# Kernel optimization log

Hardware: AMD Instinct MI355X
Metric: run time of the kernel (lower is better)

## Reference

```python
import jax, jax.numpy as jnp
import numpy as np

L, H, B = 16, 1024, 4096


def setup_inputs() -> dict:
    key = jax.random.key(0)
    k1, k2, k3, k4 = jax.random.split(key, 4)
    z = jax.random.normal(k1, (B, H), dtype=jnp.float32)
    layer_ids = jax.random.randint(k2, (B,), 0, L)
    # Module initializes weight = identity per layer; add small noise so the
    # transform is non-trivial while staying near the module's init regime.
    eye = jnp.broadcast_to(jnp.eye(H, dtype=jnp.float32), (L, H, H))
    weight = eye + 0.02 * jax.random.normal(k3, (L, H, H), dtype=jnp.float32)
    bias = 0.02 * jax.random.normal(k4, (L, H), dtype=jnp.float32)
    return {"z": z, "layer_ids": layer_ids, "weight": weight, "bias": bias}


def reference(z, layer_ids, weight, bias):
    # Faithful math: out[b] = weight[layer_ids[b]] @ z[b] + bias[layer_ids[b]].
    # Instead of materializing the gathered [B,H,H] weight tensor (as torch.bmm
    # forces), compute all-layer outputs with a grouped GEMM [B,L,H] and select.
    out_all = jnp.einsum('lij,bj->bli', weight, z)  # [B, L, H]
    out = jnp.take_along_axis(out_all, layer_ids[:, None, None], axis=1)[:, 0, :]  # [B, H]
    return out + bias[layer_ids]
```

## Files before the change

kernel.cpp:

```cpp
#include <hip/hip_runtime.h>


#define HDIM 1024
#define LNUM 16
#define BTOT 4096

constexpr int BM = 64, BN = 128, BK = 32;
constexpr int NT = HDIM / BK;
constexpr int MSLOTS = 8;

constexpr int LROW = 128;
constexpr int AOFF = 0;
constexpr int BOFF = 8192;
constexpr int BUFSZ = 24576;

typedef __attribute__((ext_vector_type(4))) float floatx4;
typedef __attribute__((ext_vector_type(2))) __fp16 cvt16x2;
typedef __attribute__((ext_vector_type(8))) _Float16 f16x8;
typedef __attribute__((ext_vector_type(2))) unsigned int uintx2;

__device__ __forceinline__ void split4(floatx4 v, uintx2& hw, uintx2& lw) {
    cvt16x2 h01 = __builtin_amdgcn_cvt_pkrtz(v[0], v[1]);
    cvt16x2 h23 = __builtin_amdgcn_cvt_pkrtz(v[2], v[3]);
    cvt16x2 l01 = __builtin_amdgcn_cvt_pkrtz(v[0] - (float)h01[0],
                                             v[1] - (float)h01[1]);
    cvt16x2 l23 = __builtin_amdgcn_cvt_pkrtz(v[2] - (float)h23[0],
                                             v[3] - (float)h23[1]);
    hw[0] = __builtin_bit_cast(unsigned int, h01);
    hw[1] = __builtin_bit_cast(unsigned int, h23);
    lw[0] = __builtin_bit_cast(unsigned int, l01);
    lw[1] = __builtin_bit_cast(unsigned int, l23);
}

__global__ __launch_bounds__(256, 3) void fused_grouped_mfma_kernel(
    const float* __restrict__ z,
    const int* __restrict__ layer_ids,
    const float* __restrict__ weight,
    const float* __restrict__ bias,
    float* __restrict__ out) {

    const int bid  = blockIdx.x;
    const int xcd  = bid & 7;
    const int slot = bid >> 3;
    const int l    = xcd + ((slot >> 6) << 3);
    const int rem  = slot & 63;
    const int my   = rem >> 3;
    const int nx   = rem & 7;
    const int n0   = nx * BN;

    const int tid  = threadIdx.x;
    const int lane = tid & 63;
    const int w    = tid >> 6;
    const int wm   = w & 1;
    const int wn   = w >> 1;

    __shared__ __align__(16) unsigned char sm[2][BUFSZ];
    __shared__ int permTile[BM];
    __shared__ int waveSums[4];

    const int4* lid4 = (const int4*)layer_ids;
    unsigned mask = 0;
#pragma unroll
    for (int q = 0; q < 4; ++q) {
        int4 v = lid4[tid * 4 + q];
        mask |= (unsigned)(v.x == l) << (4 * q)
             |  (unsigned)(v.y == l) << (4 * q + 1)
             |  (unsigned)(v.z == l) << (4 * q + 2)
             |  (unsigned)(v.w == l) << (4 * q + 3);
    }
    const int ct = __popc(mask);
    int x = ct;
#pragma unroll
    for (int o = 1; o < 64; o <<= 1) {
        int v = __shfl_up(x, o);
        if (lane >= o) x += v;
    }
    if (lane == 63) waveSums[w] = x;
    __syncthreads();
    int waveBase = 0, cnt = 0;
#pragma unroll
    for (int w2 = 0; w2 < 4; ++w2) {
        int s = waveSums[w2];
        if (w2 < w) waveBase += s;
        cnt += s;
    }
    const int et = waveBase + x - ct;

    const int kq  = tid & 7;
    const int rb  = tid >> 3;
    const int swz = (rb & 7) << 1;
    const int wA_hi = AOFF + rb * LROW + ((kq ^ swz) << 3);
    const int wA_lo = AOFF + rb * LROW + (((8 + kq) ^ swz) << 3);
    const int wB_hi = BOFF + rb * LROW + ((kq ^ swz) << 3);
    const int wB_lo = BOFF + rb * LROW + (((8 + kq) ^ swz) << 3);

    const int lr = lane & 15;
    const int ks = lane >> 4;
    const int rdA_hi = AOFF + (wm * 32 + lr) * LROW + ((ks ^ (lr & 7)) << 4);
    const int rdA_lo = AOFF + (wm * 32 + lr) * LROW + (((4 + ks) ^ (lr & 7)) << 4);
    const int rdB_hi = BOFF + (wn * 64 + lr) * LROW + ((ks ^ (lr & 7)) << 4);
    const int rdB_lo = BOFF + (wn * 64 + lr) * LROW + (((4 + ks) ^ (lr & 7)) << 4);

    const float* wBase = weight + (size_t)l * HDIM * HDIM;
    const int colBase = n0 + wn * 64 + lr;
    float bb[4];
#pragma unroll
    for (int j = 0; j < 4; ++j) bb[j] = bias[l * HDIM + colBase + j * 16];

    for (int m0 = my * BM; m0 < cnt; m0 += MSLOTS * BM) {
        __syncthreads();
        {
            unsigned m2 = mask;
            int r = et;
            while (m2) {
                int p = __ffs(m2) - 1;
                m2 &= m2 - 1;
                unsigned rr = (unsigned)(r - m0);
                if (rr < (unsigned)BM) permTile[rr] = tid * 16 + p;
                ++r;
            }
        }
        __syncthreads();

        const float* aPtr[2];
        const float* bPtr[4];
#pragma unroll
        for (int p = 0; p < 2; ++p) {
            int gm = rb + 32 * p;
            if (gm > cnt - 1 - m0) gm = cnt - 1 - m0;
            aPtr[p] = z + (size_t)permTile[gm] * HDIM + kq * 4;
        }
#pragma unroll
        for (int p = 0; p < 4; ++p)
            bPtr[p] = wBase + (size_t)(n0 + rb + 32 * p) * HDIM + kq * 4;

        floatx4 acc[2][4] = {};
        floatx4 av[2], bv[4];

        auto loadT = [&](int k0) {
#pragma unroll
            for (int p = 0; p < 2; ++p) av[p] = *(const floatx4*)(aPtr[p] + k0);
#pragma unroll
            for (int p = 0; p < 4; ++p) bv[p] = *(const floatx4*)(bPtr[p] + k0);
        };

        auto stageT = [&](unsigned char* buf) {
            uintx2 hw, lw;
#pragma unroll
            for (int p = 0; p < 2; ++p) {
                split4(av[p], hw, lw);
                *(uintx2*)(buf + wA_hi + p * 4096) = hw;
                *(uintx2*)(buf + wA_lo + p * 4096) = lw;
            }
#pragma unroll
            for (int p = 0; p < 4; ++p) {
                split4(bv[p], hw, lw);
                *(uintx2*)(buf + wB_hi + p * 4096) = hw;
                *(uintx2*)(buf + wB_lo + p * 4096) = lw;
            }
        };

        auto compute = [&](const unsigned char* buf) {
            f16x8 ah[2], al[2], bh[4], bl[4];
#pragma unroll
            for (int i = 0; i < 2; ++i) {
                ah[i] = *(const f16x8*)(buf + rdA_hi + i * 2048);
                al[i] = *(const f16x8*)(buf + rdA_lo + i * 2048);
            }
#pragma unroll
            for (int j = 0; j < 4; ++j) {
                bh[j] = *(const f16x8*)(buf + rdB_hi + j * 2048);
                bl[j] = *(const f16x8*)(buf + rdB_lo + j * 2048);
            }
#pragma unroll
            for (int i = 0; i < 2; ++i)
#pragma unroll
                for (int j = 0; j < 4; ++j) {
                    acc[i][j] = __builtin_amdgcn_mfma_f32_16x16x32_f16(
                        ah[i], bh[j], acc[i][j], 0, 0, 0);
                    acc[i][j] = __builtin_amdgcn_mfma_f32_16x16x32_f16(
                        ah[i], bl[j], acc[i][j], 0, 0, 0);
                    acc[i][j] = __builtin_amdgcn_mfma_f32_16x16x32_f16(
                        al[i], bh[j], acc[i][j], 0, 0, 0);
                }
        };

        loadT(0);
        stageT(sm[0]);
        __syncthreads();

#pragma unroll 1
        for (int t2 = 0; t2 < NT; t2 += 2) {
            loadT((t2 + 1) * BK);
            compute(sm[0]);
            stageT(sm[1]);
            __syncthreads();
            if (t2 + 2 < NT) {
                loadT((t2 + 2) * BK);
                compute(sm[1]);
                stageT(sm[0]);
                __syncthreads();
            } else {
                compute(sm[1]);
            }
        }

        const int rq = lane >> 4;
#pragma unroll
        for (int i = 0; i < 2; ++i) {
#pragma unroll
            for (int v = 0; v < 4; ++v) {
                int gm = wm * 32 + i * 16 + rq * 4 + v;
                if (m0 + gm < cnt) {
                    float* o = out + (size_t)permTile[gm] * HDIM + colBase;
#pragma unroll
                    for (int j = 0; j < 4; ++j) o[j * 16] = acc[i][j][v] + bb[j];
                }
            }
        }
    }
}

extern "C" void kernel_launch(void* const* d_in, const int* in_sizes, int n_in,
                              void* d_out, int out_size, void* d_ws, size_t ws_size,
                              hipStream_t stream) {
    const float* z = nullptr;
    const int* layer_ids = nullptr;
    const float* weight = nullptr;
    const float* bias = nullptr;
    for (int i = 0; i < n_in; ++i) {
        switch (in_sizes[i]) {
            case BTOT * HDIM:        z = (const float*)d_in[i]; break;
            case BTOT:               layer_ids = (const int*)d_in[i]; break;
            case LNUM * HDIM * HDIM: weight = (const float*)d_in[i]; break;
            case LNUM * HDIM:        bias = (const float*)d_in[i]; break;
        }
    }
    float* out = (float*)d_out;

    fused_grouped_mfma_kernel<<<dim3(1024), 256, 0, stream>>>(
        z, layer_ids, weight, bias, out);
}
```

Measured before the change: 146.1 us.

## Load MFMA operands directly from global memory, drop LDS staging and weight lo term

Removes the shared-memory double buffer and its barriers. Each lane now loads its MFMA fragments straight from global memory and converts them to fp16 in registers. The weight operand is rounded to a single fp16 value, dropping its low-order correction term, so each k-step issues two MFMAs per tile instead of three. Occupancy hint is lowered to 2. The change removes LDS traffic and synchronization, but it also loses the LDS reuse across waves, so each wave re-fetches its own A/B rows from global/L2. It also lowers accuracy, because the weight is now single-fp16 precision.

Measured after the change: 220.8 us. +51.2%, slower.

```diff
diff --git a/kernel.cpp b/kernel.cpp
--- a/kernel.cpp
+++ b/kernel.cpp
@@ -8,16 +8,12 @@
 constexpr int BM = 64, BN = 128, BK = 32;
 constexpr int NT = HDIM / BK;
 constexpr int MSLOTS = 8;
-
-constexpr int LROW = 128;
-constexpr int AOFF = 0;
-constexpr int BOFF = 8192;
-constexpr int BUFSZ = 24576;
 
 typedef __attribute__((ext_vector_type(4))) float floatx4;
 typedef __attribute__((ext_vector_type(2))) __fp16 cvt16x2;
 typedef __attribute__((ext_vector_type(8))) _Float16 f16x8;
 typedef __attribute__((ext_vector_type(2))) unsigned int uintx2;
+typedef __attribute__((ext_vector_type(4))) unsigned int uintx4;
 
 __device__ __forceinline__ void split4(floatx4 v, uintx2& hw, uintx2& lw) {
     cvt16x2 h01 = __builtin_amdgcn_cvt_pkrtz(v[0], v[1]);
@@ -32,7 +28,31 @@
     lw[1] = __builtin_bit_cast(unsigned int, l23);
 }
 
-__global__ __launch_bounds__(256, 3) void fused_grouped_mfma_kernel(
+__device__ __forceinline__ void split8(floatx4 v0, floatx4 v1,
+                                       f16x8& hi, f16x8& lo) {
+    uintx2 h0, l0, h1, l1;
+    split4(v0, h0, l0);
+    split4(v1, h1, l1);
+    uintx4 h = {h0[0], h0[1], h1[0], h1[1]};
+    uintx4 l = {l0[0], l0[1], l1[0], l1[1]};
+    hi = __builtin_bit_cast(f16x8, h);
+    lo = __builtin_bit_cast(f16x8, l);
+}
+
+__device__ __forceinline__ f16x8 cvt8_rtn(floatx4 v0, floatx4 v1) {
+    unsigned u0 = (unsigned)__builtin_bit_cast(unsigned short, (_Float16)v0[0])
+                | ((unsigned)__builtin_bit_cast(unsigned short, (_Float16)v0[1]) << 16);
+    unsigned u1 = (unsigned)__builtin_bit_cast(unsigned short, (_Float16)v0[2])
+                | ((unsigned)__builtin_bit_cast(unsigned short, (_Float16)v0[3]) << 16);
+    unsigned u2 = (unsigned)__builtin_bit_cast(unsigned short, (_Float16)v1[0])
+                | ((unsigned)__builtin_bit_cast(unsigned short, (_Float16)v1[1]) << 16);
+    unsigned u3 = (unsigned)__builtin_bit_cast(unsigned short, (_Float16)v1[2])
+                | ((unsigned)__builtin_bit_cast(unsigned short, (_Float16)v1[3]) << 16);
+    uintx4 u = {u0, u1, u2, u3};
+    return __builtin_bit_cast(f16x8, u);
+}
+
+__global__ __launch_bounds__(256, 2) void fused_direct_mfma_kernel(
     const float* __restrict__ z,
     const int* __restrict__ layer_ids,
     const float* __restrict__ weight,
@@ -54,7 +74,6 @@
     const int wm   = w & 1;
     const int wn   = w >> 1;
 
-    __shared__ __align__(16) unsigned char sm[2][BUFSZ];
     __shared__ int permTile[BM];
     __shared__ int waveSums[4];
 
@@ -86,22 +105,15 @@
     }
     const int et = waveBase + x - ct;
 
-    const int kq  = tid & 7;
-    const int rb  = tid >> 3;
-    const int swz = (rb & 7) << 1;
-    const int wA_hi = AOFF + rb * LROW + ((kq ^ swz) << 3);
-    const int wA_lo = AOFF + rb * LROW + (((8 + kq) ^ swz) << 3);
-    const int wB_hi = BOFF + rb * LROW + ((kq ^ swz) << 3);
-    const int wB_lo = BOFF + rb * LROW + (((8 + kq) ^ swz) << 3);
-
     const int lr = lane & 15;
     const int ks = lane >> 4;
-    const int rdA_hi = AOFF + (wm * 32 + lr) * LROW + ((ks ^ (lr & 7)) << 4);
-    const int rdA_lo = AOFF + (wm * 32 + lr) * LROW + (((4 + ks) ^ (lr & 7)) << 4);
-    const int rdB_hi = BOFF + (wn * 64 + lr) * LROW + ((ks ^ (lr & 7)) << 4);
-    const int rdB_lo = BOFF + (wn * 64 + lr) * LROW + (((4 + ks) ^ (lr & 7)) << 4);
-
     const float* wBase = weight + (size_t)l * HDIM * HDIM;
+
+    const float* bRow[4];
+#pragma unroll
+    for (int j = 0; j < 4; ++j)
+        bRow[j] = wBase + (size_t)(n0 + wn * 64 + j * 16 + lr) * HDIM + ks * 8;
+
     const int colBase = n0 + wn * 64 + lr;
     float bb[4];
 #pragma unroll
@@ -122,87 +134,54 @@
         }
         __syncthreads();
 
-        const float* aPtr[2];
-        const float* bPtr[4];
-#pragma unroll
-        for (int p = 0; p < 2; ++p) {
-            int gm = rb + 32 * p;
+        const float* aRow[2];
+#pragma unroll
+        for (int i = 0; i < 2; ++i) {
+            int gm = wm * 32 + i * 16 + lr;
             if (gm > cnt - 1 - m0) gm = cnt - 1 - m0;
-            aPtr[p] = z + (size_t)permTile[gm] * HDIM + kq * 4;
-        }
-#pragma unroll
-        for (int p = 0; p < 4; ++p)
-            bPtr[p] = wBase + (size_t)(n0 + rb + 32 * p) * HDIM + kq * 4;
+            aRow[i] = z + (size_t)permTile[gm] * HDIM + ks * 8;
+        }
 
         floatx4 acc[2][4] = {};
-        floatx4 av[2], bv[4];
+        floatx4 av[2][2], bv[4][2];
 
         auto loadT = [&](int k0) {
 #pragma unroll
-            for (int p = 0; p < 2; ++p) av[p] = *(const floatx4*)(aPtr[p] + k0);
-#pragma unroll
-            for (int p = 0; p < 4; ++p) bv[p] = *(const floatx4*)(bPtr[p] + k0);
+            for (int i = 0; i < 2; ++i) {
+                av[i][0] = *(const floatx4*)(aRow[i] + k0);
+                av[i][1] = *(const floatx4*)(aRow[i] + k0 + 4);
+            }
+#pragma unroll
+            for (int j = 0; j < 4; ++j) {
+                bv[j][0] = *(const floatx4*)(bRow[j] + k0);
+                bv[j][1] = *(const floatx4*)(bRow[j] + k0 + 4);
+            }
         };
 
-        auto stageT = [&](unsigned char* buf) {
-            uintx2 hw, lw;
-#pragma unroll
-            for (int p = 0; p < 2; ++p) {
-                split4(av[p], hw, lw);
-                *(uintx2*)(buf + wA_hi + p * 4096) = hw;
-                *(uintx2*)(buf + wA_lo + p * 4096) = lw;
-            }
-#pragma unroll
-            for (int p = 0; p < 4; ++p) {
-                split4(bv[p], hw, lw);
-                *(uintx2*)(buf + wB_hi + p * 4096) = hw;
-                *(uintx2*)(buf + wB_lo + p * 4096) = lw;
-            }
-        };
-
-        auto compute = [&](const unsigned char* buf) {
-            f16x8 ah[2], al[2], bh[4], bl[4];
-#pragma unroll
-            for (int i = 0; i < 2; ++i) {
-                ah[i] = *(const f16x8*)(buf + rdA_hi + i * 2048);
-                al[i] = *(const f16x8*)(buf + rdA_lo + i * 2048);
-            }
-#pragma unroll
-            for (int j = 0; j < 4; ++j) {
-                bh[j] = *(const f16x8*)(buf + rdB_hi + j * 2048);
-                bl[j] = *(const f16x8*)(buf + rdB_lo + j * 2048);
-            }
+        loadT(0);
+
+#pragma unroll 2
+        for (int t = 0; t < NT; ++t) {
+            f16x8 ah[2], al[2], bh[4];
+#pragma unroll
+            for (int i = 0; i < 2; ++i) split8(av[i][0], av[i][1], ah[i], al[i]);
+#pragma unroll
+            for (int j = 0; j < 4; ++j) bh[j] = cvt8_rtn(bv[j][0], bv[j][1]);
+
+            if (t + 1 < NT) loadT((t + 1) * BK);
+
 #pragma unroll
             for (int i = 0; i < 2; ++i)
 #pragma unroll
-                for (int j = 0; j < 4; ++j) {
+                for (int j = 0; j < 4; ++j)
                     acc[i][j] = __builtin_amdgcn_mfma_f32_16x16x32_f16(
                         ah[i], bh[j], acc[i][j], 0, 0, 0);
-                    acc[i][j] = __builtin_amdgcn_mfma_f32_16x16x32_f16(
-                        ah[i], bl[j], acc[i][j], 0, 0, 0);
+#pragma unroll
+            for (int i = 0; i < 2; ++i)
+#pragma unroll
+                for (int j = 0; j < 4; ++j)
                     acc[i][j] = __builtin_amdgcn_mfma_f32_16x16x32_f16(
                         al[i], bh[j], acc[i][j], 0, 0, 0);
-                }
-        };
-
-        loadT(0);
-        stageT(sm[0]);
-        __syncthreads();
-
-#pragma unroll 1
-        for (int t2 = 0; t2 < NT; t2 += 2) {
-            loadT((t2 + 1) * BK);
-            compute(sm[0]);
-            stageT(sm[1]);
-            __syncthreads();
-            if (t2 + 2 < NT) {
-                loadT((t2 + 2) * BK);
-                compute(sm[1]);
-                stageT(sm[0]);
-                __syncthreads();
-            } else {
-                compute(sm[1]);
-            }
         }
 
         const int rq = lane >> 4;
@@ -238,6 +217,6 @@
     }
     float* out = (float*)d_out;
 
-    fused_grouped_mfma_kernel<<<dim3(1024), 256, 0, stream>>>(
+    fused_direct_mfma_kernel<<<dim3(1024), 256, 0, stream>>>(
         z, layer_ids, weight, bias, out);
 }
```
